# Performance work log

Hardware: AMD Instinct MI355X
Metric: run time of the kernel (lower is better)

## Reference

```python
import jax, jax.numpy as jnp
import numpy as np
from jax import lax

B, CO, CI, KH, KW, H, W = 32, 128, 128, 3, 3, 56, 56
STRIDE = (1, 1)
PADDING = ((1, 1), (1, 1))


def setup_inputs() -> dict:
    key = jax.random.key(0)
    k1, k2, k3, k4 = jax.random.split(key, 4)
    inp = jax.random.normal(k1, (B, CI, H, W), dtype=jnp.float32)
    eps = jax.random.normal(k2, (B, CO, CI, KH, KW), dtype=jnp.float32)
    # reset_parameters: psi ~ U(-6, -5); mu ~ U(-stdv, stdv), stdv = 1/sqrt(CI*KH*KW)
    weight_psi = jax.random.uniform(k3, (CO, CI, KH, KW), dtype=jnp.float32,
                                    minval=-6.0, maxval=-5.0)
    stdv = 1.0 / np.sqrt(CI * KH * KW)
    weight_mu = jax.random.uniform(k4, (CO, CI, KH, KW), dtype=jnp.float32,
                                   minval=-stdv, maxval=stdv)
    return {"input": inp, "eps": eps, "weight_psi": weight_psi, "weight_mu": weight_mu}


def reference(input, eps, weight_psi, weight_mu):
    # mul_exp_add: per-sample weight = eps * exp(psi) + mu  -> [B, CO, CI, KH, KW]
    weight = eps * jnp.exp(weight_psi) + weight_mu

    # Per-example conv (torch does it via groups = bs trick); here vmap over batch.
    def conv_one(x, w):  # x: [CI,H,W], w: [CO,CI,KH,KW]
        return lax.conv_general_dilated(
            x[None], w, window_strides=STRIDE, padding=PADDING,
            dimension_numbers=("NCHW", "OIHW", "NCHW"))[0]

    out = jax.vmap(conv_one)(input, weight)  # [B, CO, H, W]
    return out
```

## Files before the change

kernel.cpp:

```cpp
#include <hip/hip_runtime.h>
#include <hip/hip_bf16.h>

#define CO    128
#define CI    128
#define NPIX  3136
#define PH    58
#define PPIX  3364
#define HPX   232
#define SROW2 144

typedef __bf16 bf16x8 __attribute__((ext_vector_type(8)));
typedef float  f32x4  __attribute__((ext_vector_type(4)));

__global__ void prep_all(const float* __restrict__ in,
                         const float* __restrict__ eps,
                         const float* __restrict__ psi,
                         const float* __restrict__ mu,
                         __bf16* __restrict__ wt,
                         __bf16* __restrict__ it) {
  __shared__ __align__(16) char smem[32256];
  const int bx = blockIdx.x, tid = threadIdx.x;

  if (bx < 2048) {
    float* Ebuf = (float*)smem;
    float* Pbuf = (float*)(smem + 9216);
    float* Mbuf = (float*)(smem + 18432);
    __bf16* Wb  = (__bf16*)(smem + 27648);
    const int idx0  = bx * 256;
    const int b     = idx0 >> 14;
    const int coci0 = idx0 & 16383;
    const f32x4* esrc = (const f32x4*)(eps + (size_t)idx0 * 9);
    const f32x4* psrc = (const f32x4*)(psi + (size_t)coci0 * 9);
    const f32x4* msrc = (const f32x4*)(mu  + (size_t)coci0 * 9);
#pragma unroll
    for (int i = 0; i < 3; ++i) {
      int j = i * 256 + tid;
      if (j < 576) {
        ((f32x4*)Ebuf)[j] = esrc[j];
        ((f32x4*)Pbuf)[j] = psrc[j];
        ((f32x4*)Mbuf)[j] = msrc[j];
      }
    }
    __syncthreads();
#pragma unroll
    for (int p = 0; p < 9; ++p) {
      float v = Ebuf[tid * 9 + p] * __expf(Pbuf[tid * 9 + p]) + Mbuf[tid * 9 + p];
      Wb[p * 256 + tid] = (__bf16)v;
    }
    __syncthreads();
    __bf16* wb = wt + (size_t)b * 9 * CO * CI + coci0;
#pragma unroll
    for (int i = 0; i < 2; ++i) {
      int s = i * 256 + tid;
      if (s < 288) {
        int p = s >> 5, j = s & 31;
        *(f32x4*)(wb + (size_t)p * CO * CI + j * 8) =
            *(const f32x4*)&Wb[p * 256 + j * 8];
      }
    }
  } else if (bx < 2504) {
    int cid = (bx - 2048) * 256 + tid;
    int pid = cid >> 4;
    int chunk = cid & 15;
    int h  = chunk >> 3;
    int c8 = chunk & 7;
    int b = pid / 228;
    int e = pid - b * 228;
    int ph, pw;
    if (e < 58)       { ph = 0;       pw = e; }
    else if (e < 116) { ph = 57;      pw = e - 58; }
    else if (e < 172) { ph = e - 115; pw = 0; }
    else              { ph = e - 171; pw = 57; }
    f32x4 z = {0.f, 0.f, 0.f, 0.f};
    *(f32x4*)&it[((size_t)(b * 2 + h) * PPIX + ph * PH + pw) * 64 + c8 * 8] = z;
  } else {
    __bf16 (*T)[136] = (__bf16(*)[136])smem;
    int tx = bx - 2504;
    int b  = tx / 49;
    int p0 = (tx - b * 49) * 64;
    const float* src = in + (size_t)b * CI * NPIX;
#pragma unroll
    for (int jj = 0; jj < 8; ++jj) {
      int c = jj * 256 + tid;
      int ci = c >> 4, xc = c & 15;
      float4 v = *(const float4*)(src + (size_t)ci * NPIX + p0 + xc * 4);
      T[xc * 4 + 0][ci] = (__bf16)v.x;
      T[xc * 4 + 1][ci] = (__bf16)v.y;
      T[xc * 4 + 2][ci] = (__bf16)v.z;
      T[xc * 4 + 3][ci] = (__bf16)v.w;
    }
    __syncthreads();
#pragma unroll
    for (int jj = 0; jj < 4; ++jj) {
      int c = jj * 256 + tid;
      int pl = c >> 4, xc = c & 15;
      int h  = xc >> 3;
      int c8 = xc & 7;
      int pix = p0 + pl;
      int oh = pix / 56, ow = pix - oh * 56;
      int ppix = (oh + 1) * PH + (ow + 1);
      *(f32x4*)&it[((size_t)(b * 2 + h) * PPIX + ppix) * 64 + c8 * 8] =
          *(const f32x4*)&T[pl][xc * 8];
    }
  }
}

__global__ __launch_bounds__(256, 4) void bconv_gemm(
    const __bf16* __restrict__ wt,
    const __bf16* __restrict__ it,
    float* __restrict__ out) {
  __shared__ __align__(16) char Bsh[HPX * SROW2];
  const int tid  = threadIdx.x;
  const int w    = tid >> 6;
  const int lane = tid & 63;
  const int quad = lane >> 4;
  const int l15  = lane & 15;

  const int lin = blockIdx.x;
  const int x   = lin & 7;
  const int j   = lin >> 3;
  const int bhi = j & 3;
  const int tile = j >> 2;
  const int b   = x + 8 * bhi;
  const int oh0 = tile * 2;

  const __bf16* hsrc0 = it + ((size_t)(b * 2 + 0) * PPIX + oh0 * PH) * 64;
  const __bf16* hsrc1 = it + ((size_t)(b * 2 + 1) * PPIX + oh0 * PH) * 64;
#pragma unroll
  for (int i = 0; i < 8; ++i) {
    int idx = i * 256 + tid;
    if (idx < HPX * 8) {
      int px = idx >> 3, sub = idx & 7;
      *(f32x4*)&Bsh[px * SROW2 + sub * 16] = *(const f32x4*)(hsrc0 + (size_t)idx * 8);
    }
  }
  __syncthreads();

  int bbase[7];
#pragma unroll
  for (int nf = 0; nf < 7; ++nf) {
    int n = nf * 16 + l15;
    int r = (n >= 56) ? 1 : 0;
    int c = n - r * 56;
    bbase[nf] = (r * PH + c) * SROW2 + quad * 16;
  }

  const int co0 = w * 32;
  const __bf16* wtb = wt + (size_t)b * 9 * CO * CI;
  const int ab0 = (co0 +      l15) * CI + quad * 8;
  const int ab1 = (co0 + 16 + l15) * CI + quad * 8;

  f32x4 acc[2][7] = {};
  bf16x8 areg[3][2];
  areg[0][0] = *(const bf16x8*)(wtb + ab0);
  areg[0][1] = *(const bf16x8*)(wtb + ab1);
  areg[1][0] = *(const bf16x8*)(wtb + 32 + ab0);
  areg[1][1] = *(const bf16x8*)(wtb + 32 + ab1);

#pragma unroll
  for (int s = 0; s < 36; ++s) {
    if (s == 18) {
      __syncthreads();
#pragma unroll
      for (int i = 0; i < 8; ++i) {
        int idx = i * 256 + tid;
        if (idx < HPX * 8) {
          int px = idx >> 3, sub = idx & 7;
          *(f32x4*)&Bsh[px * SROW2 + sub * 16] = *(const f32x4*)(hsrc1 + (size_t)idx * 8);
        }
      }
      __syncthreads();
    }
    if (s < 34) {
      const int tn  = s + 2;
      const int hn  = tn / 18;
      const int s2n = tn % 18;
      const int pn  = s2n >> 1;
      const int kkn = s2n & 1;
      const __bf16* ap = wtb + pn * (CO * CI) + hn * 64 + kkn * 32;
      areg[tn % 3][0] = *(const bf16x8*)(ap + ab0);
      areg[tn % 3][1] = *(const bf16x8*)(ap + ab1);
    }
    const int s2 = s % 18;
    const int p  = s2 >> 1;
    const int kk = s2 & 1;
    const int kh = p / 3, kw = p - kh * 3;
    const int tapb = (kh * PH + kw) * SROW2 + kk * 64;
    __builtin_amdgcn_s_setprio(1);
#pragma unroll
    for (int nf = 0; nf < 7; ++nf) {
      bf16x8 bfr = *(const bf16x8*)&Bsh[bbase[nf] + tapb];
      acc[0][nf] = __builtin_amdgcn_mfma_f32_16x16x32_bf16(areg[s % 3][0], bfr, acc[0][nf], 0, 0, 0);
      acc[1][nf] = __builtin_amdgcn_mfma_f32_16x16x32_bf16(areg[s % 3][1], bfr, acc[1][nf], 0, 0, 0);
    }
    __builtin_amdgcn_s_setprio(0);
  }

  float* ob = out + (size_t)b * CO * NPIX + oh0 * 56;
#pragma unroll
  for (int mf = 0; mf < 2; ++mf) {
#pragma unroll
    for (int nf = 0; nf < 7; ++nf) {
#pragma unroll
      for (int r = 0; r < 4; ++r) {
        int co = co0 + mf * 16 + quad * 4 + r;
        ob[(size_t)co * NPIX + nf * 16 + l15] = acc[mf][nf][r];
      }
    }
  }
}

extern "C" void kernel_launch(void* const* d_in, const int* in_sizes, int n_in,
                              void* d_out, int out_size, void* d_ws, size_t ws_size,
                              hipStream_t stream) {
  const float* inp = (const float*)d_in[0];
  const float* eps = (const float*)d_in[1];
  const float* psi = (const float*)d_in[2];
  const float* mu  = (const float*)d_in[3];

  __bf16* wt = (__bf16*)d_ws;
  __bf16* it = (__bf16*)((char*)d_ws + 9437184);

  prep_all<<<4072, 256, 0, stream>>>(inp, eps, psi, mu, wt, it);
  bconv_gemm<<<896, 256, 0, stream>>>(wt, it, (float*)d_out);
}
```

Baseline: 156.4 us.

## Enlarge conv GEMM tile to four output rows with 2x2 warp split

Each block now computes four output rows instead of two. Its four warps are arranged as two channel groups by two row pairs, and each warp holds a 64x112 accumulator tile. This halves the grid and raises reuse of both the weight fragments and the shared-memory input halo, cutting the redundant halo row loads and the weight global reads per output. In exchange each warp needs more registers (launch bounds drop to 2 blocks per CU), uses more LDS per block, and only 448 blocks are launched, which lowers occupancy and wave-level parallelism.

Result: no change. 157.4 us (+0.6%).

```diff
diff --git a/kernel.cpp b/kernel.cpp
--- a/kernel.cpp
+++ b/kernel.cpp
@@ -6,7 +6,7 @@
 #define NPIX  3136
 #define PH    58
 #define PPIX  3364
-#define HPX   232
+#define HPX4  348
 #define SROW2 144
 
 typedef __bf16 bf16x8 __attribute__((ext_vector_type(8)));
@@ -105,16 +105,18 @@
   }
 }
 
-__global__ __launch_bounds__(256, 4) void bconv_gemm(
+__global__ __launch_bounds__(256, 2) void bconv_gemm(
     const __bf16* __restrict__ wt,
     const __bf16* __restrict__ it,
     float* __restrict__ out) {
-  __shared__ __align__(16) char Bsh[HPX * SROW2];
+  __shared__ __align__(16) char Bsh[HPX4 * SROW2];
   const int tid  = threadIdx.x;
   const int w    = tid >> 6;
   const int lane = tid & 63;
   const int quad = lane >> 4;
   const int l15  = lane & 15;
+  const int cg   = w & 1;
+  const int ng   = w >> 1;
 
   const int lin = blockIdx.x;
   const int x   = lin & 7;
@@ -122,14 +124,14 @@
   const int bhi = j & 3;
   const int tile = j >> 2;
   const int b   = x + 8 * bhi;
-  const int oh0 = tile * 2;
+  const int oh0 = tile * 4;
 
   const __bf16* hsrc0 = it + ((size_t)(b * 2 + 0) * PPIX + oh0 * PH) * 64;
   const __bf16* hsrc1 = it + ((size_t)(b * 2 + 1) * PPIX + oh0 * PH) * 64;
 #pragma unroll
-  for (int i = 0; i < 8; ++i) {
+  for (int i = 0; i < 11; ++i) {
     int idx = i * 256 + tid;
-    if (idx < HPX * 8) {
+    if (idx < HPX4 * 8) {
       int px = idx >> 3, sub = idx & 7;
       *(f32x4*)&Bsh[px * SROW2 + sub * 16] = *(const f32x4*)(hsrc0 + (size_t)idx * 8);
     }
@@ -140,31 +142,34 @@
 #pragma unroll
   for (int nf = 0; nf < 7; ++nf) {
     int n = nf * 16 + l15;
-    int r = (n >= 56) ? 1 : 0;
-    int c = n - r * 56;
+    int hi = (n >= 56) ? 1 : 0;
+    int r = ng * 2 + hi;
+    int c = n - hi * 56;
     bbase[nf] = (r * PH + c) * SROW2 + quad * 16;
   }
 
-  const int co0 = w * 32;
+  const int co0 = cg * 64;
   const __bf16* wtb = wt + (size_t)b * 9 * CO * CI;
-  const int ab0 = (co0 +      l15) * CI + quad * 8;
-  const int ab1 = (co0 + 16 + l15) * CI + quad * 8;
-
-  f32x4 acc[2][7] = {};
-  bf16x8 areg[3][2];
-  areg[0][0] = *(const bf16x8*)(wtb + ab0);
-  areg[0][1] = *(const bf16x8*)(wtb + ab1);
-  areg[1][0] = *(const bf16x8*)(wtb + 32 + ab0);
-  areg[1][1] = *(const bf16x8*)(wtb + 32 + ab1);
+  int ab[4];
+#pragma unroll
+  for (int mf = 0; mf < 4; ++mf)
+    ab[mf] = (co0 + mf * 16 + l15) * CI + quad * 8;
+
+  f32x4 acc[4][7] = {};
+  bf16x8 areg[3][4];
+#pragma unroll
+  for (int mf = 0; mf < 4; ++mf) areg[0][mf] = *(const bf16x8*)(wtb + ab[mf]);
+#pragma unroll
+  for (int mf = 0; mf < 4; ++mf) areg[1][mf] = *(const bf16x8*)(wtb + 32 + ab[mf]);
 
 #pragma unroll
   for (int s = 0; s < 36; ++s) {
     if (s == 18) {
       __syncthreads();
 #pragma unroll
-      for (int i = 0; i < 8; ++i) {
+      for (int i = 0; i < 11; ++i) {
         int idx = i * 256 + tid;
-        if (idx < HPX * 8) {
+        if (idx < HPX4 * 8) {
           int px = idx >> 3, sub = idx & 7;
           *(f32x4*)&Bsh[px * SROW2 + sub * 16] = *(const f32x4*)(hsrc1 + (size_t)idx * 8);
         }
@@ -178,8 +183,9 @@
       const int pn  = s2n >> 1;
       const int kkn = s2n & 1;
       const __bf16* ap = wtb + pn * (CO * CI) + hn * 64 + kkn * 32;
-      areg[tn % 3][0] = *(const bf16x8*)(ap + ab0);
-      areg[tn % 3][1] = *(const bf16x8*)(ap + ab1);
+#pragma unroll
+      for (int mf = 0; mf < 4; ++mf)
+        areg[tn % 3][mf] = *(const bf16x8*)(ap + ab[mf]);
     }
     const int s2 = s % 18;
     const int p  = s2 >> 1;
@@ -190,15 +196,16 @@
 #pragma unroll
     for (int nf = 0; nf < 7; ++nf) {
       bf16x8 bfr = *(const bf16x8*)&Bsh[bbase[nf] + tapb];
-      acc[0][nf] = __builtin_amdgcn_mfma_f32_16x16x32_bf16(areg[s % 3][0], bfr, acc[0][nf], 0, 0, 0);
-      acc[1][nf] = __builtin_amdgcn_mfma_f32_16x16x32_bf16(areg[s % 3][1], bfr, acc[1][nf], 0, 0, 0);
+#pragma unroll
+      for (int mf = 0; mf < 4; ++mf)
+        acc[mf][nf] = __builtin_amdgcn_mfma_f32_16x16x32_bf16(areg[s % 3][mf], bfr, acc[mf][nf], 0, 0, 0);
     }
     __builtin_amdgcn_s_setprio(0);
   }
 
-  float* ob = out + (size_t)b * CO * NPIX + oh0 * 56;
-#pragma unroll
-  for (int mf = 0; mf < 2; ++mf) {
+  float* ob = out + (size_t)b * CO * NPIX + oh0 * 56 + ng * 112;
+#pragma unroll
+  for (int mf = 0; mf < 4; ++mf) {
 #pragma unroll
     for (int nf = 0; nf < 7; ++nf) {
 #pragma unroll
@@ -222,5 +229,5 @@
   __bf16* it = (__bf16*)((char*)d_ws + 9437184);
 
   prep_all<<<4072, 256, 0, stream>>>(inp, eps, psi, mu, wt, it);
-  bconv_gemm<<<896, 256, 0, stream>>>(wt, it, (float*)d_out);
+  bconv_gemm<<<448, 256, 0, stream>>>(wt, it, (float*)d_out);
 }
```

## Switch conv GEMM spatial tile from 2x56 rows to 8x8 patches

Applied to the files above, without the earlier changes.

Each conv block now covers an 8x8 output patch with a 10x10 halo instead of two full 56-wide rows, so the grid grows from 896 to 1568 blocks and per-block LDS shrinks. Launch bounds rise to 8 blocks per CU to use the smaller footprint. The intent is better occupancy and finer load balance across CUs. In exchange, halo overhead per output pixel is higher, each A fragment is reused over fewer N fragments, and output stores become 8-wide row segments rather than contiguous runs.

After: 285.6 us. +82.6%, slower.

```diff
diff --git a/kernel.cpp b/kernel.cpp
--- a/kernel.cpp
+++ b/kernel.cpp
@@ -6,7 +6,7 @@
 #define NPIX  3136
 #define PH    58
 #define PPIX  3364
-#define HPX   232
+#define HPX8  100
 #define SROW2 144
 
 typedef __bf16 bf16x8 __attribute__((ext_vector_type(8)));
@@ -105,11 +105,11 @@
   }
 }
 
-__global__ __launch_bounds__(256, 4) void bconv_gemm(
+__global__ __launch_bounds__(256, 8) void bconv_gemm(
     const __bf16* __restrict__ wt,
     const __bf16* __restrict__ it,
     float* __restrict__ out) {
-  __shared__ __align__(16) char Bsh[HPX * SROW2];
+  __shared__ __align__(16) char Bsh[HPX8 * SROW2];
   const int tid  = threadIdx.x;
   const int w    = tid >> 6;
   const int lane = tid & 63;
@@ -120,29 +120,31 @@
   const int x   = lin & 7;
   const int j   = lin >> 3;
   const int bhi = j & 3;
-  const int tile = j >> 2;
+  const int t   = j >> 2;
   const int b   = x + 8 * bhi;
-  const int oh0 = tile * 2;
-
-  const __bf16* hsrc0 = it + ((size_t)(b * 2 + 0) * PPIX + oh0 * PH) * 64;
-  const __bf16* hsrc1 = it + ((size_t)(b * 2 + 1) * PPIX + oh0 * PH) * 64;
-#pragma unroll
-  for (int i = 0; i < 8; ++i) {
+  const int th  = t / 7;
+  const int tw  = t - th * 7;
+
+  const __bf16* hsrc0 = it + ((size_t)(b * 2 + 0) * PPIX + (th * 8) * PH + tw * 8) * 64;
+  const __bf16* hsrc1 = it + ((size_t)(b * 2 + 1) * PPIX + (th * 8) * PH + tw * 8) * 64;
+#pragma unroll
+  for (int i = 0; i < 4; ++i) {
     int idx = i * 256 + tid;
-    if (idx < HPX * 8) {
+    if (idx < HPX8 * 8) {
       int px = idx >> 3, sub = idx & 7;
-      *(f32x4*)&Bsh[px * SROW2 + sub * 16] = *(const f32x4*)(hsrc0 + (size_t)idx * 8);
+      int r = px / 10, c = px - r * 10;
+      *(f32x4*)&Bsh[px * SROW2 + sub * 16] =
+          *(const f32x4*)(hsrc0 + ((size_t)r * PH + c) * 64 + sub * 8);
     }
   }
   __syncthreads();
 
-  int bbase[7];
-#pragma unroll
-  for (int nf = 0; nf < 7; ++nf) {
-    int n = nf * 16 + l15;
-    int r = (n >= 56) ? 1 : 0;
-    int c = n - r * 56;
-    bbase[nf] = (r * PH + c) * SROW2 + quad * 16;
+  int bbase[4];
+#pragma unroll
+  for (int nf = 0; nf < 4; ++nf) {
+    int orow = nf * 2 + (l15 >> 3);
+    int ocol = l15 & 7;
+    bbase[nf] = (orow * 10 + ocol) * SROW2 + quad * 16;
   }
 
   const int co0 = w * 32;
@@ -150,7 +152,7 @@
   const int ab0 = (co0 +      l15) * CI + quad * 8;
   const int ab1 = (co0 + 16 + l15) * CI + quad * 8;
 
-  f32x4 acc[2][7] = {};
+  f32x4 acc[2][4] = {};
   bf16x8 areg[3][2];
   areg[0][0] = *(const bf16x8*)(wtb + ab0);
   areg[0][1] = *(const bf16x8*)(wtb + ab1);
@@ -162,11 +164,13 @@
     if (s == 18) {
       __syncthreads();
 #pragma unroll
-      for (int i = 0; i < 8; ++i) {
+      for (int i = 0; i < 4; ++i) {
         int idx = i * 256 + tid;
-        if (idx < HPX * 8) {
+        if (idx < HPX8 * 8) {
           int px = idx >> 3, sub = idx & 7;
-          *(f32x4*)&Bsh[px * SROW2 + sub * 16] = *(const f32x4*)(hsrc1 + (size_t)idx * 8);
+          int r = px / 10, c = px - r * 10;
+          *(f32x4*)&Bsh[px * SROW2 + sub * 16] =
+              *(const f32x4*)(hsrc1 + ((size_t)r * PH + c) * 64 + sub * 8);
         }
       }
       __syncthreads();
@@ -185,10 +189,10 @@
     const int p  = s2 >> 1;
     const int kk = s2 & 1;
     const int kh = p / 3, kw = p - kh * 3;
-    const int tapb = (kh * PH + kw) * SROW2 + kk * 64;
+    const int tapb = (kh * 10 + kw) * SROW2 + kk * 64;
     __builtin_amdgcn_s_setprio(1);
 #pragma unroll
-    for (int nf = 0; nf < 7; ++nf) {
+    for (int nf = 0; nf < 4; ++nf) {
       bf16x8 bfr = *(const bf16x8*)&Bsh[bbase[nf] + tapb];
       acc[0][nf] = __builtin_amdgcn_mfma_f32_16x16x32_bf16(areg[s % 3][0], bfr, acc[0][nf], 0, 0, 0);
       acc[1][nf] = __builtin_amdgcn_mfma_f32_16x16x32_bf16(areg[s % 3][1], bfr, acc[1][nf], 0, 0, 0);
@@ -196,15 +200,17 @@
     __builtin_amdgcn_s_setprio(0);
   }
 
-  float* ob = out + (size_t)b * CO * NPIX + oh0 * 56;
+  float* ob = out + (size_t)b * CO * NPIX + (th * 8) * 56 + tw * 8;
 #pragma unroll
   for (int mf = 0; mf < 2; ++mf) {
 #pragma unroll
-    for (int nf = 0; nf < 7; ++nf) {
+    for (int nf = 0; nf < 4; ++nf) {
+      int orow = nf * 2 + (l15 >> 3);
+      int ocol = l15 & 7;
 #pragma unroll
       for (int r = 0; r < 4; ++r) {
         int co = co0 + mf * 16 + quad * 4 + r;
-        ob[(size_t)co * NPIX + nf * 16 + l15] = acc[mf][nf][r];
+        ob[(size_t)co * NPIX + orow * 56 + ocol] = acc[mf][nf][r];
       }
     }
   }
@@ -222,5 +228,5 @@
   __bf16* it = (__bf16*)((char*)d_ws + 9437184);
 
   prep_all<<<4072, 256, 0, stream>>>(inp, eps, psi, mu, wt, it);
-  bconv_gemm<<<896, 256, 0, stream>>>(wt, it, (float*)d_out);
+  bconv_gemm<<<1568, 256, 0, stream>>>(wt, it, (float*)d_out);
 }
```
